# Optimization experiments

Measured on AMD Instinct MI355X. Metric: run time of the kernel, lower is better.

## Reference

```python
import jax, jax.numpy as jnp
import numpy as np

IN_FEATURES = 256
HIDDEN_SIZE = 512
OUT_FEATURES = 256


def setup_inputs() -> dict:
    key = jax.random.key(0)
    k_x, k_w1, k_b1, k_w2, k_b2 = jax.random.split(key, 5)
    batch, seq_len = 64, 2048
    # PyTorch nn.Linear init scale ~ 1/sqrt(fan_in)
    s1 = 1.0 / np.sqrt(IN_FEATURES + HIDDEN_SIZE)
    s2 = 1.0 / np.sqrt(HIDDEN_SIZE)
    return {
        "x": jax.random.normal(k_x, (batch, seq_len, IN_FEATURES), dtype=jnp.float32),
        # W1: [hidden+in, hidden]; concat order in original is (hidden, input)
        "W1": jax.random.uniform(k_w1, (HIDDEN_SIZE + IN_FEATURES, HIDDEN_SIZE), minval=-s1, maxval=s1, dtype=jnp.float32),
        "b1": jax.random.uniform(k_b1, (HIDDEN_SIZE,), minval=-s1, maxval=s1, dtype=jnp.float32),
        "W2": jax.random.uniform(k_w2, (HIDDEN_SIZE, OUT_FEATURES), minval=-s2, maxval=s2, dtype=jnp.float32),
        "b2": jax.random.uniform(k_b2, (OUT_FEATURES,), minval=-s2, maxval=s2, dtype=jnp.float32),
    }


def reference(x, W1, b1, W2, b2):
    # x: [batch, seq, in] -> scan over seq
    batch = x.shape[0]
    # Split W1 into the hidden-part and input-part (concat order: hidden first)
    W1_h = W1[:HIDDEN_SIZE]   # [hidden, hidden]
    W1_x = W1[HIDDEN_SIZE:]   # [in, hidden]
    h0 = jnp.zeros((batch, HIDDEN_SIZE), dtype=x.dtype)

    def step(h, x_t):
        # equivalent to concat([h, x_t], -1) @ W1 + b1
        h_new = jnp.tanh(h @ W1_h + x_t @ W1_x + b1)
        y_t = h_new @ W2 + b2
        return h_new, y_t

    xs = jnp.swapaxes(x, 0, 1)              # [seq, batch, in]
    h_last, ys = jax.lax.scan(step, h0, xs)  # ys: [seq, batch, out]
    output = jnp.swapaxes(ys, 0, 1)          # [batch, seq, out]
    # original returns curr_hidden_state with leading dim 1
    return output, h_last[None, :, :]
```

## Files before the change

kernel.cpp:

```cpp
#include <hip/hip_runtime.h>
#include <math.h>


#define BB 64
#define TT 2048
#define II 256
#define HH 512
#define OO 256
#define NBLK 256
#define OUT_OFF ((size_t)BB * TT * OO)
#define NTAGS (4 * 64 * 2)

typedef unsigned long long ull;
#define F4C(v,i) ((i)==0?(v).x:((i)==1?(v).y:((i)==2?(v).z:(v).w)))

__global__ void rnn_init(int* __restrict__ tags) {
    int i = blockIdx.x * blockDim.x + threadIdx.x;
    if (i < NTAGS) tags[i] = 0;
}

__device__ inline float4 ld_h4(const ull* p) {
    ull a = __hip_atomic_load(p,     __ATOMIC_RELAXED, __HIP_MEMORY_SCOPE_AGENT);
    ull b = __hip_atomic_load(p + 1, __ATOMIC_RELAXED, __HIP_MEMORY_SCOPE_AGENT);
    float2 lo = __builtin_bit_cast(float2, a);
    float2 hi = __builtin_bit_cast(float2, b);
    return make_float4(lo.x, lo.y, hi.x, hi.y);
}

__global__ __launch_bounds__(256, 1) void rnn_persist(
    const float* __restrict__ x, const float* __restrict__ W1,
    const float* __restrict__ b1, const float* __restrict__ W2,
    const float* __restrict__ b2, float* __restrict__ out,
    int* __restrict__ tags, float* __restrict__ hbuf)
{
    __shared__ float sc_h[16 * 8 * 32];
    __shared__ float sc_y[16 * 4 * 32];

    const int tid = threadIdx.x;
    const int blk = blockIdx.x;
    const int bi  = blk >> 6;
    const int cj  = blk & 63;
    const int R0  = bi << 4;
    const int C0  = cj << 3;
    const int O0  = cj << 2;

    const int g  = tid & 31;
    const int r2 = tid >> 5;
    const int oc = tid & 7;
    const int yi = tid - 128, yo = yi & 3, yrow = yi >> 2;

    float w1r[6][4][8];
    #pragma unroll
    for (int j = 0; j < 6; ++j)
        #pragma unroll
        for (int i = 0; i < 4; ++i) {
            const float* wp = W1 + (size_t)(j * 128 + (g << 2) + i) * HH + C0;
            float4 a = *(const float4*)wp;
            float4 b = *(const float4*)(wp + 4);
            w1r[j][i][0] = a.x; w1r[j][i][1] = a.y; w1r[j][i][2] = a.z; w1r[j][i][3] = a.w;
            w1r[j][i][4] = b.x; w1r[j][i][5] = b.y; w1r[j][i][6] = b.z; w1r[j][i][7] = b.w;
        }
    float w2r[4][4][4];
    #pragma unroll
    for (int j = 0; j < 4; ++j)
        #pragma unroll
        for (int i = 0; i < 4; ++i) {
            float4 a = *(const float4*)(W2 + (size_t)(j * 128 + (g << 2) + i) * OO + O0);
            w2r[j][i][0] = a.x; w2r[j][i][1] = a.y; w2r[j][i][2] = a.z; w2r[j][i][3] = a.w;
        }
    const float b1v = (tid < 128) ? b1[C0 + oc] : 0.f;
    const float b2v = (tid >= 128 && tid < 192) ? b2[O0 + yo] : 0.f;

    ull* hb[2] = { (ull*)hbuf, (ull*)(hbuf + (size_t)BB * HH) };
    int* mytag = &tags[((bi << 6) + cj) * 2];
    const int* ptag = &tags[((bi << 6) + (tid >> 1)) * 2 + (tid & 1)];

    for (int t = 0; t < TT; ++t) {
        float4 xreg[2][2];
        #pragma unroll
        for (int rr = 0; rr < 2; ++rr)
            #pragma unroll
            for (int jx = 0; jx < 2; ++jx)
                xreg[rr][jx] = *(const float4*)&x[((size_t)(R0 + r2 + (rr << 3)) * TT + t) * II
                                                  + jx * 128 + (g << 2)];
        float4 hreg[2][4];
        if (t > 0) {
            if (tid < 128)
                while (__hip_atomic_load(ptag, __ATOMIC_RELAXED,
                                         __HIP_MEMORY_SCOPE_AGENT) < t) {}
            __syncthreads();
            const ull* hsrc = hb[t & 1];
            #pragma unroll
            for (int rr = 0; rr < 2; ++rr) {
                const ull* rp = hsrc + (size_t)(R0 + r2 + (rr << 3)) * (HH / 2) + (g << 1);
                #pragma unroll
                for (int j = 0; j < 4; ++j)
                    hreg[rr][j] = ld_h4(rp + j * 64);
            }
        } else {
            #pragma unroll
            for (int rr = 0; rr < 2; ++rr)
                #pragma unroll
                for (int j = 0; j < 4; ++j)
                    hreg[rr][j] = make_float4(0.f, 0.f, 0.f, 0.f);
            __syncthreads();
        }

        float pa[2][8];
        float py[2][4];
        #pragma unroll
        for (int rr = 0; rr < 2; ++rr) {
            #pragma unroll
            for (int c = 0; c < 8; ++c) pa[rr][c] = 0.f;
            #pragma unroll
            for (int o = 0; o < 4; ++o) py[rr][o] = 0.f;
        }
        #pragma unroll
        for (int rr = 0; rr < 2; ++rr) {
            #pragma unroll
            for (int j = 0; j < 6; ++j) {
                float4 vv = (j < 4) ? hreg[rr][j] : xreg[rr][j - 4];
                #pragma unroll
                for (int i = 0; i < 4; ++i) {
                    const float vi = F4C(vv, i);
                    #pragma unroll
                    for (int c = 0; c < 8; ++c)
                        pa[rr][c] = fmaf(vi, w1r[j][i][c], pa[rr][c]);
                }
            }
            if (t > 0) {
                #pragma unroll
                for (int j = 0; j < 4; ++j) {
                    float4 vv = hreg[rr][j];
                    #pragma unroll
                    for (int i = 0; i < 4; ++i) {
                        const float vi = F4C(vv, i);
                        #pragma unroll
                        for (int o = 0; o < 4; ++o)
                            py[rr][o] = fmaf(vi, w2r[j][i][o], py[rr][o]);
                    }
                }
            }
        }
        #pragma unroll
        for (int rr = 0; rr < 2; ++rr) {
            const int row = r2 + (rr << 3);
            #pragma unroll
            for (int c = 0; c < 8; ++c)
                sc_h[((row << 3) + c) * 32 + (g ^ (c << 2))] = pa[rr][c];
            if (t > 0)
                #pragma unroll
                for (int o = 0; o < 4; ++o)
                    sc_y[((row << 2) + o) * 32 + (g ^ (o << 2))] = py[rr][o];
        }
        __syncthreads();

        if (tid < 128) {
            float s = 0.f;
            #pragma unroll
            for (int j = 0; j < 8; ++j) {
                float4 q = *(const float4*)&sc_h[(tid << 5) + ((j << 2) ^ (oc << 2))];
                s += (q.x + q.y) + (q.z + q.w);
            }
            float hnew = tanhf(s + b1v);
            float* hdst = (float*)hb[(t + 1) & 1];
            __hip_atomic_store(&hdst[(size_t)(R0 + (tid >> 3)) * HH + C0 + oc], hnew,
                               __ATOMIC_RELAXED, __HIP_MEMORY_SCOPE_AGENT);
            if (t == TT - 1)
                out[OUT_OFF + (size_t)(R0 + (tid >> 3)) * HH + C0 + oc] = hnew;
            asm volatile("s_waitcnt vmcnt(0)" ::: "memory");
            if ((tid & 63) == 0)
                __hip_atomic_store(&mytag[tid >> 6], t + 1,
                                   __ATOMIC_RELAXED, __HIP_MEMORY_SCOPE_AGENT);
        } else if (tid < 192 && t > 0) {
            float s = 0.f;
            #pragma unroll
            for (int j = 0; j < 8; ++j) {
                float4 q = *(const float4*)&sc_y[(yi << 5) + ((j << 2) ^ (yo << 2))];
                s += (q.x + q.y) + (q.z + q.w);
            }
            out[((size_t)(R0 + yrow) * TT + (t - 1)) * OO + O0 + yo] = s + b2v;
        }
    }

    if (tid < 128)
        while (__hip_atomic_load(ptag, __ATOMIC_RELAXED,
                                 __HIP_MEMORY_SCOPE_AGENT) < TT) {}
    __syncthreads();
    {
        float4 hreg[2][4];
        const ull* hsrc = hb[TT & 1];
        #pragma unroll
        for (int rr = 0; rr < 2; ++rr) {
            const ull* rp = hsrc + (size_t)(R0 + r2 + (rr << 3)) * (HH / 2) + (g << 1);
            #pragma unroll
            for (int j = 0; j < 4; ++j)
                hreg[rr][j] = ld_h4(rp + j * 64);
        }
        float py[2][4];
        #pragma unroll
        for (int rr = 0; rr < 2; ++rr) {
            #pragma unroll
            for (int o = 0; o < 4; ++o) py[rr][o] = 0.f;
            #pragma unroll
            for (int j = 0; j < 4; ++j) {
                float4 vv = hreg[rr][j];
                #pragma unroll
                for (int i = 0; i < 4; ++i) {
                    const float vi = F4C(vv, i);
                    #pragma unroll
                    for (int o = 0; o < 4; ++o)
                        py[rr][o] = fmaf(vi, w2r[j][i][o], py[rr][o]);
                }
            }
            const int row = r2 + (rr << 3);
            #pragma unroll
            for (int o = 0; o < 4; ++o)
                sc_y[((row << 2) + o) * 32 + (g ^ (o << 2))] = py[rr][o];
        }
        __syncthreads();
        if (tid >= 128 && tid < 192) {
            float s = 0.f;
            #pragma unroll
            for (int j = 0; j < 8; ++j) {
                float4 q = *(const float4*)&sc_y[(yi << 5) + ((j << 2) ^ (yo << 2))];
                s += (q.x + q.y) + (q.z + q.w);
            }
            out[((size_t)(R0 + yrow) * TT + (TT - 1)) * OO + O0 + yo] = s + b2v;
        }
    }
}

extern "C" void kernel_launch(void* const* d_in, const int* in_sizes, int n_in,
                              void* d_out, int out_size, void* d_ws, size_t ws_size,
                              hipStream_t stream) {
    const float* x  = (const float*)d_in[0];
    const float* W1 = (const float*)d_in[1];
    const float* b1 = (const float*)d_in[2];
    const float* W2 = (const float*)d_in[3];
    const float* b2 = (const float*)d_in[4];
    float* out = (float*)d_out;

    int*   tags = (int*)d_ws;
    float* hbuf = (float*)((char*)d_ws + 4096);

    rnn_init<<<dim3(2), dim3(256), 0, stream>>>(tags);
    rnn_persist<<<dim3(NBLK), dim3(256), 0, stream>>>(x, W1, b1, W2, b2, out,
                                                      tags, hbuf);
}
```

Baseline: 12.44 ms.

## Replace tag flags with step-tagged hidden values and warp-shuffle reductions

Each hidden value is now stored as a 64-bit word that pairs the float with its timestep. Consumers spin directly on the data words, which removes the separate tag array, the s_waitcnt before publishing, and the block-wide barriers. The cross-lane partial sums now use __shfl_xor instead of shared-memory scratch plus __syncthreads. This shortens the per-step critical path of the recurrence, but it doubles hidden-state traffic (8 bytes per element) and every thread polls the memory it reads.

Measured after the change: 14.68 ms. 1.18x slower.

```diff
diff --git a/kernel.cpp b/kernel.cpp
--- a/kernel.cpp
+++ b/kernel.cpp
@@ -9,33 +9,23 @@
 #define OO 256
 #define NBLK 256
 #define OUT_OFF ((size_t)BB * TT * OO)
-#define NTAGS (4 * 64 * 2)
 
 typedef unsigned long long ull;
 #define F4C(v,i) ((i)==0?(v).x:((i)==1?(v).y:((i)==2?(v).z:(v).w)))
 
-__global__ void rnn_init(int* __restrict__ tags) {
+__device__ inline float u2f(unsigned u) { return __builtin_bit_cast(float, u); }
+
+__global__ void rnn_init(ull* __restrict__ hbuf) {
     int i = blockIdx.x * blockDim.x + threadIdx.x;
-    if (i < NTAGS) tags[i] = 0;
-}
-
-__device__ inline float4 ld_h4(const ull* p) {
-    ull a = __hip_atomic_load(p,     __ATOMIC_RELAXED, __HIP_MEMORY_SCOPE_AGENT);
-    ull b = __hip_atomic_load(p + 1, __ATOMIC_RELAXED, __HIP_MEMORY_SCOPE_AGENT);
-    float2 lo = __builtin_bit_cast(float2, a);
-    float2 hi = __builtin_bit_cast(float2, b);
-    return make_float4(lo.x, lo.y, hi.x, hi.y);
+    hbuf[i] = 0ull;
 }
 
 __global__ __launch_bounds__(256, 1) void rnn_persist(
     const float* __restrict__ x, const float* __restrict__ W1,
     const float* __restrict__ b1, const float* __restrict__ W2,
     const float* __restrict__ b2, float* __restrict__ out,
-    int* __restrict__ tags, float* __restrict__ hbuf)
+    ull* __restrict__ hbuf)
 {
-    __shared__ float sc_h[16 * 8 * 32];
-    __shared__ float sc_y[16 * 4 * 32];
-
     const int tid = threadIdx.x;
     const int blk = blockIdx.x;
     const int bi  = blk >> 6;
@@ -46,8 +36,6 @@
 
     const int g  = tid & 31;
     const int r2 = tid >> 5;
-    const int oc = tid & 7;
-    const int yi = tid - 128, yo = yi & 3, yrow = yi >> 2;
 
     float w1r[6][4][8];
     #pragma unroll
@@ -68,12 +56,11 @@
             float4 a = *(const float4*)(W2 + (size_t)(j * 128 + (g << 2) + i) * OO + O0);
             w2r[j][i][0] = a.x; w2r[j][i][1] = a.y; w2r[j][i][2] = a.z; w2r[j][i][3] = a.w;
         }
-    const float b1v = (tid < 128) ? b1[C0 + oc] : 0.f;
-    const float b2v = (tid >= 128 && tid < 192) ? b2[O0 + yo] : 0.f;
-
-    ull* hb[2] = { (ull*)hbuf, (ull*)(hbuf + (size_t)BB * HH) };
-    int* mytag = &tags[((bi << 6) + cj) * 2];
-    const int* ptag = &tags[((bi << 6) + (tid >> 1)) * 2 + (tid & 1)];
+    const float b1v = b1[C0 + (g & 7)];
+    const float b2v = b2[O0 + (g & 3)];
+
+    ull* hb[2] = { hbuf, hbuf + (size_t)BB * HH };
+    const int row0 = R0 + r2;
 
     for (int t = 0; t < TT; ++t) {
         float4 xreg[2][2];
@@ -81,29 +68,33 @@
         for (int rr = 0; rr < 2; ++rr)
             #pragma unroll
             for (int jx = 0; jx < 2; ++jx)
-                xreg[rr][jx] = *(const float4*)&x[((size_t)(R0 + r2 + (rr << 3)) * TT + t) * II
+                xreg[rr][jx] = *(const float4*)&x[((size_t)(row0 + (rr << 3)) * TT + t) * II
                                                   + jx * 128 + (g << 2)];
+
         float4 hreg[2][4];
-        if (t > 0) {
-            if (tid < 128)
-                while (__hip_atomic_load(ptag, __ATOMIC_RELAXED,
-                                         __HIP_MEMORY_SCOPE_AGENT) < t) {}
-            __syncthreads();
+        {
             const ull* hsrc = hb[t & 1];
-            #pragma unroll
-            for (int rr = 0; rr < 2; ++rr) {
-                const ull* rp = hsrc + (size_t)(R0 + r2 + (rr << 3)) * (HH / 2) + (g << 1);
-                #pragma unroll
-                for (int j = 0; j < 4; ++j)
-                    hreg[rr][j] = ld_h4(rp + j * 64);
-            }
-        } else {
-            #pragma unroll
-            for (int rr = 0; rr < 2; ++rr)
-                #pragma unroll
-                for (int j = 0; j < 4; ++j)
-                    hreg[rr][j] = make_float4(0.f, 0.f, 0.f, 0.f);
-            __syncthreads();
+            int bad;
+            do {
+                bad = 0;
+                #pragma unroll
+                for (int rr = 0; rr < 2; ++rr)
+                    #pragma unroll
+                    for (int j = 0; j < 4; ++j) {
+                        const ull* bp = hsrc + (size_t)(row0 + (rr << 3)) * HH
+                                             + (j << 7) + (g << 2);
+                        ull p0 = __hip_atomic_load(bp + 0, __ATOMIC_RELAXED, __HIP_MEMORY_SCOPE_AGENT);
+                        ull p1 = __hip_atomic_load(bp + 1, __ATOMIC_RELAXED, __HIP_MEMORY_SCOPE_AGENT);
+                        ull p2 = __hip_atomic_load(bp + 2, __ATOMIC_RELAXED, __HIP_MEMORY_SCOPE_AGENT);
+                        ull p3 = __hip_atomic_load(bp + 3, __ATOMIC_RELAXED, __HIP_MEMORY_SCOPE_AGENT);
+                        bad |= (int)((unsigned)(p0 >> 32) != (unsigned)t);
+                        bad |= (int)((unsigned)(p1 >> 32) != (unsigned)t);
+                        bad |= (int)((unsigned)(p2 >> 32) != (unsigned)t);
+                        bad |= (int)((unsigned)(p3 >> 32) != (unsigned)t);
+                        hreg[rr][j] = make_float4(u2f((unsigned)p0), u2f((unsigned)p1),
+                                                  u2f((unsigned)p2), u2f((unsigned)p3));
+                    }
+            } while (__builtin_expect(bad != 0, 0));
         }
 
         float pa[2][8];
@@ -142,61 +133,83 @@
                 }
             }
         }
-        #pragma unroll
-        for (int rr = 0; rr < 2; ++rr) {
-            const int row = r2 + (rr << 3);
-            #pragma unroll
-            for (int c = 0; c < 8; ++c)
-                sc_h[((row << 3) + c) * 32 + (g ^ (c << 2))] = pa[rr][c];
-            if (t > 0)
-                #pragma unroll
-                for (int o = 0; o < 4; ++o)
-                    sc_y[((row << 2) + o) * 32 + (g ^ (o << 2))] = py[rr][o];
-        }
-        __syncthreads();
-
-        if (tid < 128) {
-            float s = 0.f;
-            #pragma unroll
-            for (int j = 0; j < 8; ++j) {
-                float4 q = *(const float4*)&sc_h[(tid << 5) + ((j << 2) ^ (oc << 2))];
-                s += (q.x + q.y) + (q.z + q.w);
-            }
-            float hnew = tanhf(s + b1v);
-            float* hdst = (float*)hb[(t + 1) & 1];
-            __hip_atomic_store(&hdst[(size_t)(R0 + (tid >> 3)) * HH + C0 + oc], hnew,
+
+        #pragma unroll
+        for (int rr = 0; rr < 2; ++rr)
+            #pragma unroll
+            for (int c = 0; c < 8; ++c) {
+                float v = pa[rr][c];
+                v += __shfl_xor(v, 1);  v += __shfl_xor(v, 2);
+                v += __shfl_xor(v, 4);  v += __shfl_xor(v, 8);
+                v += __shfl_xor(v, 16);
+                pa[rr][c] = v;
+            }
+        if (t > 0) {
+            #pragma unroll
+            for (int rr = 0; rr < 2; ++rr)
+                #pragma unroll
+                for (int o = 0; o < 4; ++o) {
+                    float v = py[rr][o];
+                    v += __shfl_xor(v, 1);  v += __shfl_xor(v, 2);
+                    v += __shfl_xor(v, 4);  v += __shfl_xor(v, 8);
+                    v += __shfl_xor(v, 16);
+                    py[rr][o] = v;
+                }
+        }
+
+        if (g < 16) {
+            float hsum = pa[0][0];
+            #pragma unroll
+            for (int rr = 0; rr < 2; ++rr)
+                #pragma unroll
+                for (int c = 0; c < 8; ++c)
+                    if (g == ((rr << 3) | c)) hsum = pa[rr][c];
+            float hv = tanhf(hsum + b1v);
+            const int row = row0 + (g & 8);
+            ull pk = (ull)__builtin_bit_cast(unsigned, hv) | ((ull)(unsigned)(t + 1) << 32);
+            __hip_atomic_store(&hb[(t + 1) & 1][(size_t)row * HH + C0 + (g & 7)], pk,
                                __ATOMIC_RELAXED, __HIP_MEMORY_SCOPE_AGENT);
             if (t == TT - 1)
-                out[OUT_OFF + (size_t)(R0 + (tid >> 3)) * HH + C0 + oc] = hnew;
-            asm volatile("s_waitcnt vmcnt(0)" ::: "memory");
-            if ((tid & 63) == 0)
-                __hip_atomic_store(&mytag[tid >> 6], t + 1,
-                                   __ATOMIC_RELAXED, __HIP_MEMORY_SCOPE_AGENT);
-        } else if (tid < 192 && t > 0) {
-            float s = 0.f;
-            #pragma unroll
-            for (int j = 0; j < 8; ++j) {
-                float4 q = *(const float4*)&sc_y[(yi << 5) + ((j << 2) ^ (yo << 2))];
-                s += (q.x + q.y) + (q.z + q.w);
-            }
-            out[((size_t)(R0 + yrow) * TT + (t - 1)) * OO + O0 + yo] = s + b2v;
+                out[OUT_OFF + (size_t)row * HH + C0 + (g & 7)] = hv;
+        }
+        if (t > 0 && g >= 16 && g < 24) {
+            const int q = g & 7;
+            float ysum = py[0][0];
+            #pragma unroll
+            for (int rr = 0; rr < 2; ++rr)
+                #pragma unroll
+                for (int o = 0; o < 4; ++o)
+                    if (q == ((rr << 2) | o)) ysum = py[rr][o];
+            const int row = row0 + ((q >> 2) << 3);
+            out[((size_t)row * TT + (t - 1)) * OO + O0 + (q & 3)] = ysum + b2v;
         }
     }
 
-    if (tid < 128)
-        while (__hip_atomic_load(ptag, __ATOMIC_RELAXED,
-                                 __HIP_MEMORY_SCOPE_AGENT) < TT) {}
-    __syncthreads();
     {
         float4 hreg[2][4];
         const ull* hsrc = hb[TT & 1];
-        #pragma unroll
-        for (int rr = 0; rr < 2; ++rr) {
-            const ull* rp = hsrc + (size_t)(R0 + r2 + (rr << 3)) * (HH / 2) + (g << 1);
-            #pragma unroll
-            for (int j = 0; j < 4; ++j)
-                hreg[rr][j] = ld_h4(rp + j * 64);
-        }
+        int bad;
+        do {
+            bad = 0;
+            #pragma unroll
+            for (int rr = 0; rr < 2; ++rr)
+                #pragma unroll
+                for (int j = 0; j < 4; ++j) {
+                    const ull* bp = hsrc + (size_t)(row0 + (rr << 3)) * HH
+                                         + (j << 7) + (g << 2);
+                    ull p0 = __hip_atomic_load(bp + 0, __ATOMIC_RELAXED, __HIP_MEMORY_SCOPE_AGENT);
+                    ull p1 = __hip_atomic_load(bp + 1, __ATOMIC_RELAXED, __HIP_MEMORY_SCOPE_AGENT);
+                    ull p2 = __hip_atomic_load(bp + 2, __ATOMIC_RELAXED, __HIP_MEMORY_SCOPE_AGENT);
+                    ull p3 = __hip_atomic_load(bp + 3, __ATOMIC_RELAXED, __HIP_MEMORY_SCOPE_AGENT);
+                    bad |= (int)((unsigned)(p0 >> 32) != (unsigned)TT);
+                    bad |= (int)((unsigned)(p1 >> 32) != (unsigned)TT);
+                    bad |= (int)((unsigned)(p2 >> 32) != (unsigned)TT);
+                    bad |= (int)((unsigned)(p3 >> 32) != (unsigned)TT);
+                    hreg[rr][j] = make_float4(u2f((unsigned)p0), u2f((unsigned)p1),
+                                              u2f((unsigned)p2), u2f((unsigned)p3));
+                }
+        } while (__builtin_expect(bad != 0, 0));
+
         float py[2][4];
         #pragma unroll
         for (int rr = 0; rr < 2; ++rr) {
@@ -213,20 +226,27 @@
                         py[rr][o] = fmaf(vi, w2r[j][i][o], py[rr][o]);
                 }
             }
-            const int row = r2 + (rr << 3);
-            #pragma unroll
-            for (int o = 0; o < 4; ++o)
-                sc_y[((row << 2) + o) * 32 + (g ^ (o << 2))] = py[rr][o];
-        }
-        __syncthreads();
-        if (tid >= 128 && tid < 192) {
-            float s = 0.f;
-            #pragma unroll
-            for (int j = 0; j < 8; ++j) {
-                float4 q = *(const float4*)&sc_y[(yi << 5) + ((j << 2) ^ (yo << 2))];
-                s += (q.x + q.y) + (q.z + q.w);
-            }
-            out[((size_t)(R0 + yrow) * TT + (TT - 1)) * OO + O0 + yo] = s + b2v;
+        }
+        #pragma unroll
+        for (int rr = 0; rr < 2; ++rr)
+            #pragma unroll
+            for (int o = 0; o < 4; ++o) {
+                float v = py[rr][o];
+                v += __shfl_xor(v, 1);  v += __shfl_xor(v, 2);
+                v += __shfl_xor(v, 4);  v += __shfl_xor(v, 8);
+                v += __shfl_xor(v, 16);
+                py[rr][o] = v;
+            }
+        if (g >= 16 && g < 24) {
+            const int q = g & 7;
+            float ysum = py[0][0];
+            #pragma unroll
+            for (int rr = 0; rr < 2; ++rr)
+                #pragma unroll
+                for (int o = 0; o < 4; ++o)
+                    if (q == ((rr << 2) | o)) ysum = py[rr][o];
+            const int row = row0 + ((q >> 2) << 3);
+            out[((size_t)row * TT + (TT - 1)) * OO + O0 + (q & 3)] = ysum + b2v;
         }
     }
 }
@@ -241,10 +261,8 @@
     const float* b2 = (const float*)d_in[4];
     float* out = (float*)d_out;
 
-    int*   tags = (int*)d_ws;
-    float* hbuf = (float*)((char*)d_ws + 4096);
-
-    rnn_init<<<dim3(2), dim3(256), 0, stream>>>(tags);
-    rnn_persist<<<dim3(NBLK), dim3(256), 0, stream>>>(x, W1, b1, W2, b2, out,
-                                                      tags, hbuf);
+    ull* hbuf = (ull*)d_ws;
+
+    rnn_init<<<dim3(256), dim3(256), 0, stream>>>(hbuf);
+    rnn_persist<<<dim3(NBLK), dim3(256), 0, stream>>>(x, W1, b1, W2, b2, out, hbuf);
 }
```

## Restructure persistent RNN to 64 blocks with shuffle reductions and LDS-staged state

Applied to the files above, without the earlier changes.

Cuts the persistent grid from 256 to 64 blocks, so each block computes 32 hidden and 16 output columns for 16 batch rows. The hidden state and input are staged in shared memory, and partial sums are reduced with butterfly lane shuffles instead of a shared-memory scratch pass. The next timestep's x is prefetched into registers, and stores are packed in pairs. Fewer blocks means fewer tags to poll and less cross-block sync traffic, but each block does about four times the FMA work per step, and the 192 weight floats per thread raise register pressure.

Result: slower. 37.16 ms (+198.6%).

```diff
diff --git a/kernel.cpp b/kernel.cpp
--- a/kernel.cpp
+++ b/kernel.cpp
@@ -7,24 +7,26 @@
 #define II 256
 #define HH 512
 #define OO 256
-#define NBLK 256
+#define NBLK 64
 #define OUT_OFF ((size_t)BB * TT * OO)
-#define NTAGS (4 * 64 * 2)
+#define LDV 776
 
 typedef unsigned long long ull;
 #define F4C(v,i) ((i)==0?(v).x:((i)==1?(v).y:((i)==2?(v).z:(v).w)))
 
+#define HALVE(arr, SZ, DIST) { \
+    const bool hi_ = (g & (DIST)) != 0; \
+    _Pragma("unroll") \
+    for (int i_ = 0; i_ < (SZ)/2; ++i_) { \
+        float lo_ = arr[i_], hh_ = arr[i_ + (SZ)/2]; \
+        float sent_ = hi_ ? lo_ : hh_; \
+        float recv_ = __shfl_xor(sent_, (DIST)); \
+        arr[i_] = (hi_ ? hh_ : lo_) + recv_; \
+    } }
+
 __global__ void rnn_init(int* __restrict__ tags) {
     int i = blockIdx.x * blockDim.x + threadIdx.x;
-    if (i < NTAGS) tags[i] = 0;
-}
-
-__device__ inline float4 ld_h4(const ull* p) {
-    ull a = __hip_atomic_load(p,     __ATOMIC_RELAXED, __HIP_MEMORY_SCOPE_AGENT);
-    ull b = __hip_atomic_load(p + 1, __ATOMIC_RELAXED, __HIP_MEMORY_SCOPE_AGENT);
-    float2 lo = __builtin_bit_cast(float2, a);
-    float2 hi = __builtin_bit_cast(float2, b);
-    return make_float4(lo.x, lo.y, hi.x, hi.y);
+    tags[i] = 0;
 }
 
 __global__ __launch_bounds__(256, 1) void rnn_persist(
@@ -33,201 +35,197 @@
     const float* __restrict__ b2, float* __restrict__ out,
     int* __restrict__ tags, float* __restrict__ hbuf)
 {
-    __shared__ float sc_h[16 * 8 * 32];
-    __shared__ float sc_y[16 * 4 * 32];
+    __shared__ float v_s[16 * LDV];
 
     const int tid = threadIdx.x;
     const int blk = blockIdx.x;
-    const int bi  = blk >> 6;
-    const int cj  = blk & 63;
-    const int R0  = bi << 4;
-    const int C0  = cj << 3;
-    const int O0  = cj << 2;
-
-    const int g  = tid & 31;
-    const int r2 = tid >> 5;
-    const int oc = tid & 7;
-    const int yi = tid - 128, yo = yi & 3, yrow = yi >> 2;
-
-    float w1r[6][4][8];
+    const int grp = blk & 3;
+    const int cb  = blk >> 2;
+    const int R0  = grp << 4;
+    const int C0  = cb << 5;
+    const int O0  = cb << 4;
+
+    const int g  = tid & 15;
+    const int cg = (tid >> 4) & 7;
+    const int rp = tid >> 7;
+
+    float4 w1r[12][4];
     #pragma unroll
-    for (int j = 0; j < 6; ++j)
-        #pragma unroll
-        for (int i = 0; i < 4; ++i) {
-            const float* wp = W1 + (size_t)(j * 128 + (g << 2) + i) * HH + C0;
-            float4 a = *(const float4*)wp;
-            float4 b = *(const float4*)(wp + 4);
-            w1r[j][i][0] = a.x; w1r[j][i][1] = a.y; w1r[j][i][2] = a.z; w1r[j][i][3] = a.w;
-            w1r[j][i][4] = b.x; w1r[j][i][5] = b.y; w1r[j][i][6] = b.z; w1r[j][i][7] = b.w;
-        }
-    float w2r[4][4][4];
+    for (int j = 0; j < 12; ++j)
+        #pragma unroll
+        for (int i = 0; i < 4; ++i)
+            w1r[j][i] = *(const float4*)&W1[(size_t)(j * 64 + (g << 2) + i) * HH
+                                            + C0 + (cg << 2)];
+    float2 w2r[8][4];
     #pragma unroll
-    for (int j = 0; j < 4; ++j)
-        #pragma unroll
-        for (int i = 0; i < 4; ++i) {
-            float4 a = *(const float4*)(W2 + (size_t)(j * 128 + (g << 2) + i) * OO + O0);
-            w2r[j][i][0] = a.x; w2r[j][i][1] = a.y; w2r[j][i][2] = a.z; w2r[j][i][3] = a.w;
-        }
-    const float b1v = (tid < 128) ? b1[C0 + oc] : 0.f;
-    const float b2v = (tid >= 128 && tid < 192) ? b2[O0 + yo] : 0.f;
+    for (int j = 0; j < 8; ++j)
+        #pragma unroll
+        for (int i = 0; i < 4; ++i)
+            w2r[j][i] = *(const float2*)&W2[(size_t)(j * 64 + (g << 2) + i) * OO
+                                            + O0 + (cg << 1)];
+    const float2 b1v = *(const float2*)&b1[C0 + (cg << 2) + ((g & 1) << 1)];
+    const float  b2v = b2[O0 + (cg << 1) + (g & 1)];
 
     ull* hb[2] = { (ull*)hbuf, (ull*)(hbuf + (size_t)BB * HH) };
-    int* mytag = &tags[((bi << 6) + cj) * 2];
-    const int* ptag = &tags[((bi << 6) + (tid >> 1)) * 2 + (tid & 1)];
+
+    const int orow = (rp << 3) + (g >> 1);
+    const int hcol = C0 + (cg << 2) + ((g & 1) << 1);
+    const int ycol = O0 + (cg << 1) + (g & 1);
+
+    float4 xr[4];
+    #pragma unroll
+    for (int m = 0; m < 4; ++m) {
+        int idx = (m << 8) + tid;
+        xr[m] = *(const float4*)&x[((size_t)(R0 + (idx >> 6)) * TT + 0) * II
+                                   + ((idx & 63) << 2)];
+    }
 
     for (int t = 0; t < TT; ++t) {
-        float4 xreg[2][2];
-        #pragma unroll
-        for (int rr = 0; rr < 2; ++rr)
-            #pragma unroll
-            for (int jx = 0; jx < 2; ++jx)
-                xreg[rr][jx] = *(const float4*)&x[((size_t)(R0 + r2 + (rr << 3)) * TT + t) * II
-                                                  + jx * 128 + (g << 2)];
-        float4 hreg[2][4];
         if (t > 0) {
-            if (tid < 128)
-                while (__hip_atomic_load(ptag, __ATOMIC_RELAXED,
+            if (tid < 64) {
+                const int* tp = &tags[((grp + ((tid >> 2) << 2)) << 2) + (tid & 3)];
+                while (__hip_atomic_load(tp, __ATOMIC_RELAXED,
                                          __HIP_MEMORY_SCOPE_AGENT) < t) {}
-            __syncthreads();
+            }
+        }
+        __syncthreads();
+
+        #pragma unroll
+        for (int m = 0; m < 4; ++m) {
+            int idx = (m << 8) + tid;
+            *(float4*)&v_s[(idx >> 6) * LDV + 512 + ((idx & 63) << 2)] = xr[m];
+        }
+        if (t > 0) {
             const ull* hsrc = hb[t & 1];
             #pragma unroll
-            for (int rr = 0; rr < 2; ++rr) {
-                const ull* rp = hsrc + (size_t)(R0 + r2 + (rr << 3)) * (HH / 2) + (g << 1);
-                #pragma unroll
-                for (int j = 0; j < 4; ++j)
-                    hreg[rr][j] = ld_h4(rp + j * 64);
+            for (int half = 0; half < 2; ++half) {
+                ull hl[8];
+                #pragma unroll
+                for (int m = 0; m < 8; ++m) {
+                    int idx = (((half << 3) + m) << 8) + tid;
+                    hl[m] = __hip_atomic_load(
+                        &hsrc[(size_t)(R0 + (idx >> 8)) * (HH / 2) + (idx & 255)],
+                        __ATOMIC_RELAXED, __HIP_MEMORY_SCOPE_AGENT);
+                }
+                #pragma unroll
+                for (int m = 0; m < 8; ++m) {
+                    int idx = (((half << 3) + m) << 8) + tid;
+                    *(ull*)&v_s[(idx >> 8) * LDV + ((idx & 255) << 1)] = hl[m];
+                }
             }
         } else {
             #pragma unroll
-            for (int rr = 0; rr < 2; ++rr)
-                #pragma unroll
-                for (int j = 0; j < 4; ++j)
-                    hreg[rr][j] = make_float4(0.f, 0.f, 0.f, 0.f);
-            __syncthreads();
-        }
-
-        float pa[2][8];
-        float py[2][4];
-        #pragma unroll
-        for (int rr = 0; rr < 2; ++rr) {
-            #pragma unroll
-            for (int c = 0; c < 8; ++c) pa[rr][c] = 0.f;
-            #pragma unroll
-            for (int o = 0; o < 4; ++o) py[rr][o] = 0.f;
-        }
-        #pragma unroll
-        for (int rr = 0; rr < 2; ++rr) {
-            #pragma unroll
-            for (int j = 0; j < 6; ++j) {
-                float4 vv = (j < 4) ? hreg[rr][j] : xreg[rr][j - 4];
+            for (int m = 0; m < 8; ++m) {
+                int idx = (m << 8) + tid;
+                *(float4*)&v_s[(idx >> 7) * LDV + ((idx & 127) << 2)] =
+                    make_float4(0.f, 0.f, 0.f, 0.f);
+            }
+        }
+        __syncthreads();
+
+        float pa[32];
+        float py[16];
+        #pragma unroll
+        for (int i = 0; i < 32; ++i) pa[i] = 0.f;
+        #pragma unroll
+        for (int i = 0; i < 16; ++i) py[i] = 0.f;
+        #pragma unroll
+        for (int rr = 0; rr < 8; ++rr) {
+            const float* vrow = v_s + ((rp << 3) + rr) * LDV + (g << 2);
+            #pragma unroll
+            for (int j = 0; j < 12; ++j) {
+                float4 vv = *(const float4*)(vrow + (j << 6));
                 #pragma unroll
                 for (int i = 0; i < 4; ++i) {
                     const float vi = F4C(vv, i);
-                    #pragma unroll
-                    for (int c = 0; c < 8; ++c)
-                        pa[rr][c] = fmaf(vi, w1r[j][i][c], pa[rr][c]);
-                }
-            }
-            if (t > 0) {
-                #pragma unroll
-                for (int j = 0; j < 4; ++j) {
-                    float4 vv = hreg[rr][j];
-                    #pragma unroll
-                    for (int i = 0; i < 4; ++i) {
-                        const float vi = F4C(vv, i);
-                        #pragma unroll
-                        for (int o = 0; o < 4; ++o)
-                            py[rr][o] = fmaf(vi, w2r[j][i][o], py[rr][o]);
+                    pa[(rr << 2) + 0] = fmaf(vi, w1r[j][i].x, pa[(rr << 2) + 0]);
+                    pa[(rr << 2) + 1] = fmaf(vi, w1r[j][i].y, pa[(rr << 2) + 1]);
+                    pa[(rr << 2) + 2] = fmaf(vi, w1r[j][i].z, pa[(rr << 2) + 2]);
+                    pa[(rr << 2) + 3] = fmaf(vi, w1r[j][i].w, pa[(rr << 2) + 3]);
+                    if (j < 8) {
+                        py[(rr << 1) + 0] = fmaf(vi, w2r[j][i].x, py[(rr << 1) + 0]);
+                        py[(rr << 1) + 1] = fmaf(vi, w2r[j][i].y, py[(rr << 1) + 1]);
                     }
                 }
             }
         }
-        #pragma unroll
-        for (int rr = 0; rr < 2; ++rr) {
-            const int row = r2 + (rr << 3);
-            #pragma unroll
-            for (int c = 0; c < 8; ++c)
-                sc_h[((row << 3) + c) * 32 + (g ^ (c << 2))] = pa[rr][c];
-            if (t > 0)
-                #pragma unroll
-                for (int o = 0; o < 4; ++o)
-                    sc_y[((row << 2) + o) * 32 + (g ^ (o << 2))] = py[rr][o];
-        }
-        __syncthreads();
-
-        if (tid < 128) {
-            float s = 0.f;
-            #pragma unroll
-            for (int j = 0; j < 8; ++j) {
-                float4 q = *(const float4*)&sc_h[(tid << 5) + ((j << 2) ^ (oc << 2))];
-                s += (q.x + q.y) + (q.z + q.w);
-            }
-            float hnew = tanhf(s + b1v);
-            float* hdst = (float*)hb[(t + 1) & 1];
-            __hip_atomic_store(&hdst[(size_t)(R0 + (tid >> 3)) * HH + C0 + oc], hnew,
+
+        HALVE(pa, 32, 8); HALVE(pa, 16, 4); HALVE(pa, 8, 2); HALVE(pa, 4, 1);
+        {
+            float hv0 = tanhf(pa[0] + b1v.x);
+            float hv1 = tanhf(pa[1] + b1v.y);
+            ull pk = (ull)__builtin_bit_cast(unsigned, hv0)
+                   | ((ull)__builtin_bit_cast(unsigned, hv1) << 32);
+            __hip_atomic_store(&hb[(t + 1) & 1][((size_t)(R0 + orow) * HH + hcol) >> 1],
+                               pk, __ATOMIC_RELAXED, __HIP_MEMORY_SCOPE_AGENT);
+            if (t == TT - 1) {
+                out[OUT_OFF + (size_t)(R0 + orow) * HH + hcol]     = hv0;
+                out[OUT_OFF + (size_t)(R0 + orow) * HH + hcol + 1] = hv1;
+            }
+        }
+        asm volatile("s_waitcnt vmcnt(0)" ::: "memory");
+        if ((tid & 63) == 0)
+            __hip_atomic_store(&tags[(blk << 2) + (tid >> 6)], t + 1,
                                __ATOMIC_RELAXED, __HIP_MEMORY_SCOPE_AGENT);
-            if (t == TT - 1)
-                out[OUT_OFF + (size_t)(R0 + (tid >> 3)) * HH + C0 + oc] = hnew;
-            asm volatile("s_waitcnt vmcnt(0)" ::: "memory");
-            if ((tid & 63) == 0)
-                __hip_atomic_store(&mytag[tid >> 6], t + 1,
-                                   __ATOMIC_RELAXED, __HIP_MEMORY_SCOPE_AGENT);
-        } else if (tid < 192 && t > 0) {
-            float s = 0.f;
-            #pragma unroll
-            for (int j = 0; j < 8; ++j) {
-                float4 q = *(const float4*)&sc_y[(yi << 5) + ((j << 2) ^ (yo << 2))];
-                s += (q.x + q.y) + (q.z + q.w);
-            }
-            out[((size_t)(R0 + yrow) * TT + (t - 1)) * OO + O0 + yo] = s + b2v;
-        }
-    }
-
-    if (tid < 128)
-        while (__hip_atomic_load(ptag, __ATOMIC_RELAXED,
+
+        HALVE(py, 16, 8); HALVE(py, 8, 4); HALVE(py, 4, 2); HALVE(py, 2, 1);
+        if (t > 0)
+            out[((size_t)(R0 + orow) * TT + (t - 1)) * OO + ycol] = py[0] + b2v;
+
+        if (t + 1 < TT) {
+            #pragma unroll
+            for (int m = 0; m < 4; ++m) {
+                int idx = (m << 8) + tid;
+                xr[m] = *(const float4*)&x[((size_t)(R0 + (idx >> 6)) * TT + (t + 1)) * II
+                                           + ((idx & 63) << 2)];
+            }
+        }
+    }
+
+    if (tid < 64) {
+        const int* tp = &tags[((grp + ((tid >> 2) << 2)) << 2) + (tid & 3)];
+        while (__hip_atomic_load(tp, __ATOMIC_RELAXED,
                                  __HIP_MEMORY_SCOPE_AGENT) < TT) {}
+    }
     __syncthreads();
     {
-        float4 hreg[2][4];
         const ull* hsrc = hb[TT & 1];
         #pragma unroll
-        for (int rr = 0; rr < 2; ++rr) {
-            const ull* rp = hsrc + (size_t)(R0 + r2 + (rr << 3)) * (HH / 2) + (g << 1);
-            #pragma unroll
-            for (int j = 0; j < 4; ++j)
-                hreg[rr][j] = ld_h4(rp + j * 64);
-        }
-        float py[2][4];
-        #pragma unroll
-        for (int rr = 0; rr < 2; ++rr) {
-            #pragma unroll
-            for (int o = 0; o < 4; ++o) py[rr][o] = 0.f;
-            #pragma unroll
-            for (int j = 0; j < 4; ++j) {
-                float4 vv = hreg[rr][j];
+        for (int half = 0; half < 2; ++half) {
+            ull hl[8];
+            #pragma unroll
+            for (int m = 0; m < 8; ++m) {
+                int idx = (((half << 3) + m) << 8) + tid;
+                hl[m] = __hip_atomic_load(
+                    &hsrc[(size_t)(R0 + (idx >> 8)) * (HH / 2) + (idx & 255)],
+                    __ATOMIC_RELAXED, __HIP_MEMORY_SCOPE_AGENT);
+            }
+            #pragma unroll
+            for (int m = 0; m < 8; ++m) {
+                int idx = (((half << 3) + m) << 8) + tid;
+                *(ull*)&v_s[(idx >> 8) * LDV + ((idx & 255) << 1)] = hl[m];
+            }
+        }
+        __syncthreads();
+        float py[16];
+        #pragma unroll
+        for (int i = 0; i < 16; ++i) py[i] = 0.f;
+        #pragma unroll
+        for (int rr = 0; rr < 8; ++rr) {
+            const float* vrow = v_s + ((rp << 3) + rr) * LDV + (g << 2);
+            #pragma unroll
+            for (int j = 0; j < 8; ++j) {
+                float4 vv = *(const float4*)(vrow + (j << 6));
                 #pragma unroll
                 for (int i = 0; i < 4; ++i) {
                     const float vi = F4C(vv, i);
-                    #pragma unroll
-                    for (int o = 0; o < 4; ++o)
-                        py[rr][o] = fmaf(vi, w2r[j][i][o], py[rr][o]);
-                }
-            }
-            const int row = r2 + (rr << 3);
-            #pragma unroll
-            for (int o = 0; o < 4; ++o)
-                sc_y[((row << 2) + o) * 32 + (g ^ (o << 2))] = py[rr][o];
-        }
-        __syncthreads();
-        if (tid >= 128 && tid < 192) {
-            float s = 0.f;
-            #pragma unroll
-            for (int j = 0; j < 8; ++j) {
-                float4 q = *(const float4*)&sc_y[(yi << 5) + ((j << 2) ^ (yo << 2))];
-                s += (q.x + q.y) + (q.z + q.w);
-            }
-            out[((size_t)(R0 + yrow) * TT + (TT - 1)) * OO + O0 + yo] = s + b2v;
-        }
+                    py[(rr << 1) + 0] = fmaf(vi, w2r[j][i].x, py[(rr << 1) + 0]);
+                    py[(rr << 1) + 1] = fmaf(vi, w2r[j][i].y, py[(rr << 1) + 1]);
+                }
+            }
+        }
+        HALVE(py, 16, 8); HALVE(py, 8, 4); HALVE(py, 4, 2); HALVE(py, 2, 1);
+        out[((size_t)(R0 + orow) * TT + (TT - 1)) * OO + ycol] = py[0] + b2v;
     }
 }
 
@@ -244,7 +242,7 @@
     int*   tags = (int*)d_ws;
     float* hbuf = (float*)((char*)d_ws + 4096);
 
-    rnn_init<<<dim3(2), dim3(256), 0, stream>>>(tags);
+    rnn_init<<<dim3(1), dim3(256), 0, stream>>>(tags);
     rnn_persist<<<dim3(NBLK), dim3(256), 0, stream>>>(x, W1, b1, W2, b2, out,
                                                       tags, hbuf);
 }
```

## Stage hidden state through LDS with coalesced loads and prefetch next x

Applied to the files above, without the earlier changes.

Each block now loads the full 16-row hidden state from global into a padded shared-memory tile with coalesced 64-bit atomic loads, replacing per-thread scattered strided loads. The x-contribution FMAs run before the tag spin-wait, and x for the next timestep is prefetched after the barrier, so input work overlaps the inter-block synchronization latency. The cost is an extra shared-memory tile, one more barrier per step, and LDS reads in the inner FMA loop.

After: 20.73 ms. 1.67x slower.

```diff
diff --git a/kernel.cpp b/kernel.cpp
--- a/kernel.cpp
+++ b/kernel.cpp
@@ -9,22 +9,14 @@
 #define OO 256
 #define NBLK 256
 #define OUT_OFF ((size_t)BB * TT * OO)
-#define NTAGS (4 * 64 * 2)
+#define LDV 528
 
 typedef unsigned long long ull;
 #define F4C(v,i) ((i)==0?(v).x:((i)==1?(v).y:((i)==2?(v).z:(v).w)))
 
 __global__ void rnn_init(int* __restrict__ tags) {
     int i = blockIdx.x * blockDim.x + threadIdx.x;
-    if (i < NTAGS) tags[i] = 0;
-}
-
-__device__ inline float4 ld_h4(const ull* p) {
-    ull a = __hip_atomic_load(p,     __ATOMIC_RELAXED, __HIP_MEMORY_SCOPE_AGENT);
-    ull b = __hip_atomic_load(p + 1, __ATOMIC_RELAXED, __HIP_MEMORY_SCOPE_AGENT);
-    float2 lo = __builtin_bit_cast(float2, a);
-    float2 hi = __builtin_bit_cast(float2, b);
-    return make_float4(lo.x, lo.y, hi.x, hi.y);
+    if (i < 2 * NBLK) tags[i] = 0;
 }
 
 __global__ __launch_bounds__(256, 1) void rnn_persist(
@@ -33,6 +25,7 @@
     const float* __restrict__ b2, float* __restrict__ out,
     int* __restrict__ tags, float* __restrict__ hbuf)
 {
+    __shared__ float v_s[16 * LDV];
     __shared__ float sc_h[16 * 8 * 32];
     __shared__ float sc_y[16 * 4 * 32];
 
@@ -47,7 +40,7 @@
     const int g  = tid & 31;
     const int r2 = tid >> 5;
     const int oc = tid & 7;
-    const int yi = tid - 128, yo = yi & 3, yrow = yi >> 2;
+    const int yi = tid - 128;
 
     float w1r[6][4][8];
     #pragma unroll
@@ -69,43 +62,26 @@
             w2r[j][i][0] = a.x; w2r[j][i][1] = a.y; w2r[j][i][2] = a.z; w2r[j][i][3] = a.w;
         }
     const float b1v = (tid < 128) ? b1[C0 + oc] : 0.f;
-    const float b2v = (tid >= 128 && tid < 192) ? b2[O0 + yo] : 0.f;
-
-    ull* hb[2] = { (ull*)hbuf, (ull*)(hbuf + (size_t)BB * HH) };
-    int* mytag = &tags[((bi << 6) + cj) * 2];
-    const int* ptag = &tags[((bi << 6) + (tid >> 1)) * 2 + (tid & 1)];
+    const float b2v = (tid >= 128 && tid < 192) ? b2[O0 + (yi & 3)] : 0.f;
+
+    float* hb[2] = { hbuf, hbuf + (size_t)BB * HH };
+
+    #pragma unroll
+    for (int m = 0; m < 8; ++m) {
+        int idx = (m << 8) + tid;
+        *(float4*)&v_s[(idx >> 7) * LDV + ((idx & 127) << 2)] =
+            make_float4(0.f, 0.f, 0.f, 0.f);
+    }
+    float4 xreg[2][2];
+    #pragma unroll
+    for (int rr = 0; rr < 2; ++rr)
+        #pragma unroll
+        for (int jx = 0; jx < 2; ++jx)
+            xreg[rr][jx] = *(const float4*)&x[((size_t)(R0 + r2 + (rr << 3)) * TT + 0) * II
+                                              + (jx << 7) + (g << 2)];
+    __syncthreads();
 
     for (int t = 0; t < TT; ++t) {
-        float4 xreg[2][2];
-        #pragma unroll
-        for (int rr = 0; rr < 2; ++rr)
-            #pragma unroll
-            for (int jx = 0; jx < 2; ++jx)
-                xreg[rr][jx] = *(const float4*)&x[((size_t)(R0 + r2 + (rr << 3)) * TT + t) * II
-                                                  + jx * 128 + (g << 2)];
-        float4 hreg[2][4];
-        if (t > 0) {
-            if (tid < 128)
-                while (__hip_atomic_load(ptag, __ATOMIC_RELAXED,
-                                         __HIP_MEMORY_SCOPE_AGENT) < t) {}
-            __syncthreads();
-            const ull* hsrc = hb[t & 1];
-            #pragma unroll
-            for (int rr = 0; rr < 2; ++rr) {
-                const ull* rp = hsrc + (size_t)(R0 + r2 + (rr << 3)) * (HH / 2) + (g << 1);
-                #pragma unroll
-                for (int j = 0; j < 4; ++j)
-                    hreg[rr][j] = ld_h4(rp + j * 64);
-            }
-        } else {
-            #pragma unroll
-            for (int rr = 0; rr < 2; ++rr)
-                #pragma unroll
-                for (int j = 0; j < 4; ++j)
-                    hreg[rr][j] = make_float4(0.f, 0.f, 0.f, 0.f);
-            __syncthreads();
-        }
-
         float pa[2][8];
         float py[2][4];
         #pragma unroll
@@ -116,45 +92,81 @@
             for (int o = 0; o < 4; ++o) py[rr][o] = 0.f;
         }
         #pragma unroll
-        for (int rr = 0; rr < 2; ++rr) {
-            #pragma unroll
-            for (int j = 0; j < 6; ++j) {
-                float4 vv = (j < 4) ? hreg[rr][j] : xreg[rr][j - 4];
+        for (int rr = 0; rr < 2; ++rr)
+            #pragma unroll
+            for (int jx = 0; jx < 2; ++jx) {
+                float4 vv = xreg[rr][jx];
                 #pragma unroll
                 for (int i = 0; i < 4; ++i) {
                     const float vi = F4C(vv, i);
                     #pragma unroll
                     for (int c = 0; c < 8; ++c)
+                        pa[rr][c] = fmaf(vi, w1r[4 + jx][i][c], pa[rr][c]);
+                }
+            }
+        if (t > 0 && tid < 128) {
+            const int* tp = &tags[((bi << 6) + (tid >> 1)) * 2 + (tid & 1)];
+            while (__hip_atomic_load(tp, __ATOMIC_RELAXED,
+                                     __HIP_MEMORY_SCOPE_AGENT) < t) {}
+        }
+        __syncthreads();
+        if (t > 0) {
+            const ull* hsrc = (const ull*)hb[t & 1];
+            #pragma unroll
+            for (int half = 0; half < 2; ++half) {
+                ull hl[8];
+                #pragma unroll
+                for (int m = 0; m < 8; ++m) {
+                    int idx = (((half << 3) + m) << 8) + tid;
+                    hl[m] = __hip_atomic_load(
+                        &hsrc[(size_t)(R0 + (idx >> 8)) * (HH / 2) + (idx & 255)],
+                        __ATOMIC_RELAXED, __HIP_MEMORY_SCOPE_AGENT);
+                }
+                #pragma unroll
+                for (int m = 0; m < 8; ++m) {
+                    int idx = (((half << 3) + m) << 8) + tid;
+                    *(ull*)&v_s[(idx >> 8) * LDV + ((idx & 255) << 1)] = hl[m];
+                }
+            }
+        }
+        __syncthreads();
+        if (t + 1 < TT) {
+            #pragma unroll
+            for (int rr = 0; rr < 2; ++rr)
+                #pragma unroll
+                for (int jx = 0; jx < 2; ++jx)
+                    xreg[rr][jx] = *(const float4*)&x[((size_t)(R0 + r2 + (rr << 3)) * TT
+                                                      + (t + 1)) * II + (jx << 7) + (g << 2)];
+        }
+        #pragma unroll
+        for (int rr = 0; rr < 2; ++rr) {
+            const float* vrow = v_s + (r2 + (rr << 3)) * LDV + (g << 2);
+            #pragma unroll
+            for (int j = 0; j < 4; ++j) {
+                float4 vv = *(const float4*)(vrow + (j << 7));
+                #pragma unroll
+                for (int i = 0; i < 4; ++i) {
+                    const float vi = F4C(vv, i);
+                    #pragma unroll
+                    for (int c = 0; c < 8; ++c)
                         pa[rr][c] = fmaf(vi, w1r[j][i][c], pa[rr][c]);
-                }
-            }
-            if (t > 0) {
-                #pragma unroll
-                for (int j = 0; j < 4; ++j) {
-                    float4 vv = hreg[rr][j];
-                    #pragma unroll
-                    for (int i = 0; i < 4; ++i) {
-                        const float vi = F4C(vv, i);
-                        #pragma unroll
-                        for (int o = 0; o < 4; ++o)
-                            py[rr][o] = fmaf(vi, w2r[j][i][o], py[rr][o]);
-                    }
-                }
-            }
-        }
-        #pragma unroll
-        for (int rr = 0; rr < 2; ++rr) {
-            const int row = r2 + (rr << 3);
+                    #pragma unroll
+                    for (int o = 0; o < 4; ++o)
+                        py[rr][o] = fmaf(vi, w2r[j][i][o], py[rr][o]);
+                }
+            }
+        }
+        #pragma unroll
+        for (int rr = 0; rr < 2; ++rr) {
+            const int row16 = r2 + (rr << 3);
             #pragma unroll
             for (int c = 0; c < 8; ++c)
-                sc_h[((row << 3) + c) * 32 + (g ^ (c << 2))] = pa[rr][c];
-            if (t > 0)
-                #pragma unroll
-                for (int o = 0; o < 4; ++o)
-                    sc_y[((row << 2) + o) * 32 + (g ^ (o << 2))] = py[rr][o];
-        }
-        __syncthreads();
-
+                sc_h[(((row16 << 3) + c) << 5) + (g ^ (c << 2))] = pa[rr][c];
+            #pragma unroll
+            for (int o = 0; o < 4; ++o)
+                sc_y[(((row16 << 2) + o) << 5) + (g ^ (o << 2))] = py[rr][o];
+        }
+        __syncthreads();
         if (tid < 128) {
             float s = 0.f;
             #pragma unroll
@@ -162,49 +174,60 @@
                 float4 q = *(const float4*)&sc_h[(tid << 5) + ((j << 2) ^ (oc << 2))];
                 s += (q.x + q.y) + (q.z + q.w);
             }
-            float hnew = tanhf(s + b1v);
-            float* hdst = (float*)hb[(t + 1) & 1];
-            __hip_atomic_store(&hdst[(size_t)(R0 + (tid >> 3)) * HH + C0 + oc], hnew,
-                               __ATOMIC_RELAXED, __HIP_MEMORY_SCOPE_AGENT);
+            float hv = tanhf(s + b1v);
+            __hip_atomic_store(&hb[(t + 1) & 1][(size_t)(R0 + (tid >> 3)) * HH + C0 + oc],
+                               hv, __ATOMIC_RELAXED, __HIP_MEMORY_SCOPE_AGENT);
             if (t == TT - 1)
-                out[OUT_OFF + (size_t)(R0 + (tid >> 3)) * HH + C0 + oc] = hnew;
+                out[OUT_OFF + (size_t)(R0 + (tid >> 3)) * HH + C0 + oc] = hv;
             asm volatile("s_waitcnt vmcnt(0)" ::: "memory");
             if ((tid & 63) == 0)
-                __hip_atomic_store(&mytag[tid >> 6], t + 1,
+                __hip_atomic_store(&tags[(blk << 1) + (tid >> 6)], t + 1,
                                    __ATOMIC_RELAXED, __HIP_MEMORY_SCOPE_AGENT);
         } else if (tid < 192 && t > 0) {
             float s = 0.f;
             #pragma unroll
             for (int j = 0; j < 8; ++j) {
-                float4 q = *(const float4*)&sc_y[(yi << 5) + ((j << 2) ^ (yo << 2))];
+                float4 q = *(const float4*)&sc_y[(yi << 5) + ((j << 2) ^ ((yi & 3) << 2))];
                 s += (q.x + q.y) + (q.z + q.w);
             }
-            out[((size_t)(R0 + yrow) * TT + (t - 1)) * OO + O0 + yo] = s + b2v;
-        }
-    }
-
-    if (tid < 128)
-        while (__hip_atomic_load(ptag, __ATOMIC_RELAXED,
+            out[((size_t)(R0 + (yi >> 2)) * TT + (t - 1)) * OO + O0 + (yi & 3)] = s + b2v;
+        }
+    }
+
+    if (tid < 128) {
+        const int* tp = &tags[((bi << 6) + (tid >> 1)) * 2 + (tid & 1)];
+        while (__hip_atomic_load(tp, __ATOMIC_RELAXED,
                                  __HIP_MEMORY_SCOPE_AGENT) < TT) {}
+    }
     __syncthreads();
     {
-        float4 hreg[2][4];
-        const ull* hsrc = hb[TT & 1];
-        #pragma unroll
-        for (int rr = 0; rr < 2; ++rr) {
-            const ull* rp = hsrc + (size_t)(R0 + r2 + (rr << 3)) * (HH / 2) + (g << 1);
-            #pragma unroll
-            for (int j = 0; j < 4; ++j)
-                hreg[rr][j] = ld_h4(rp + j * 64);
-        }
+        const ull* hsrc = (const ull*)hb[TT & 1];
+        #pragma unroll
+        for (int half = 0; half < 2; ++half) {
+            ull hl[8];
+            #pragma unroll
+            for (int m = 0; m < 8; ++m) {
+                int idx = (((half << 3) + m) << 8) + tid;
+                hl[m] = __hip_atomic_load(
+                    &hsrc[(size_t)(R0 + (idx >> 8)) * (HH / 2) + (idx & 255)],
+                    __ATOMIC_RELAXED, __HIP_MEMORY_SCOPE_AGENT);
+            }
+            #pragma unroll
+            for (int m = 0; m < 8; ++m) {
+                int idx = (((half << 3) + m) << 8) + tid;
+                *(ull*)&v_s[(idx >> 8) * LDV + ((idx & 255) << 1)] = hl[m];
+            }
+        }
+        __syncthreads();
         float py[2][4];
         #pragma unroll
         for (int rr = 0; rr < 2; ++rr) {
             #pragma unroll
             for (int o = 0; o < 4; ++o) py[rr][o] = 0.f;
+            const float* vrow = v_s + (r2 + (rr << 3)) * LDV + (g << 2);
             #pragma unroll
             for (int j = 0; j < 4; ++j) {
-                float4 vv = hreg[rr][j];
+                float4 vv = *(const float4*)(vrow + (j << 7));
                 #pragma unroll
                 for (int i = 0; i < 4; ++i) {
                     const float vi = F4C(vv, i);
@@ -213,20 +236,20 @@
                         py[rr][o] = fmaf(vi, w2r[j][i][o], py[rr][o]);
                 }
             }
-            const int row = r2 + (rr << 3);
+            const int row16 = r2 + (rr << 3);
             #pragma unroll
             for (int o = 0; o < 4; ++o)
-                sc_y[((row << 2) + o) * 32 + (g ^ (o << 2))] = py[rr][o];
+                sc_y[(((row16 << 2) + o) << 5) + (g ^ (o << 2))] = py[rr][o];
         }
         __syncthreads();
         if (tid >= 128 && tid < 192) {
             float s = 0.f;
             #pragma unroll
             for (int j = 0; j < 8; ++j) {
-                float4 q = *(const float4*)&sc_y[(yi << 5) + ((j << 2) ^ (yo << 2))];
+                float4 q = *(const float4*)&sc_y[(yi << 5) + ((j << 2) ^ ((yi & 3) << 2))];
                 s += (q.x + q.y) + (q.z + q.w);
             }
-            out[((size_t)(R0 + yrow) * TT + (TT - 1)) * OO + O0 + yo] = s + b2v;
+            out[((size_t)(R0 + (yi >> 2)) * TT + (TT - 1)) * OO + O0 + (yi & 3)] = s + b2v;
         }
     }
 }
```
